# Kernel optimization log

Measured on AMD Instinct MI355X. Metric: run time of the kernel, lower is better.

## Reference

```python
import jax, jax.numpy as jnp
import numpy as np

EMBED_DIM = 1024
NUM_HEADS = 16
HEAD_DIM = EMBED_DIM // NUM_HEADS
SCALE = float(np.sqrt(HEAD_DIM))


def setup_inputs() -> dict:
    key = jax.random.key(0)
    ks = jax.random.split(key, 7)
    B, S, E = 2, 2048, EMBED_DIM
    query = jax.random.normal(ks[0], (B, S, E), dtype=jnp.float32)
    key_t = jax.random.normal(ks[1], (B, S, E), dtype=jnp.float32)
    value = jax.random.normal(ks[2], (B, S, E), dtype=jnp.float32)
    # nn.Linear(E, E, bias=False): weight shape (out, in); y = x @ W.T
    std = 1.0 / np.sqrt(E)
    Wq = jax.random.uniform(ks[3], (E, E), jnp.float32, -std, std)
    Wk = jax.random.uniform(ks[4], (E, E), jnp.float32, -std, std)
    Wv = jax.random.uniform(ks[5], (E, E), jnp.float32, -std, std)
    Wo = jax.random.uniform(ks[6], (E, E), jnp.float32, -std, std)
    return {"query": query, "key": key_t, "value": value,
            "Wq": Wq, "Wk": Wk, "Wv": Wv, "Wo": Wo}


def reference(query, key, value, Wq, Wk, Wv, Wo):
    B, S, E = query.shape
    H, D = NUM_HEADS, HEAD_DIM
    q = (query @ Wq.T).reshape(B, S, H, D).transpose(0, 2, 1, 3)  # [B,H,S,D]
    k = (key @ Wk.T).reshape(B, S, H, D).transpose(0, 2, 1, 3)
    v = (value @ Wv.T).reshape(B, S, H, D).transpose(0, 2, 1, 3)
    scores = jnp.einsum('bhqd,bhkd->bhqk', q, k) / SCALE  # [B,H,S,S]
    attn = jax.nn.softmax(scores, axis=-1)
    out = jnp.einsum('bhqk,bhkd->bhqd', attn, v)  # [B,H,S,D]
    out = out.transpose(0, 2, 1, 3).reshape(B, S, E)
    return out @ Wo.T
```

## Files before the change

### kernel.cpp

```cpp
#include <hip/hip_runtime.h>
#include <hip/hip_bf16.h>
#include <math.h>

typedef float f32x4 __attribute__((ext_vector_type(4)));
typedef __bf16 bf16x8 __attribute__((ext_vector_type(8)));
typedef unsigned short u16;
typedef u16 u16x8 __attribute__((ext_vector_type(8)));
typedef u16 u16x4 __attribute__((ext_vector_type(4)));
typedef unsigned ui32x4 __attribute__((ext_vector_type(4)));

__device__ __forceinline__ u16 f2bf(float f) {
    unsigned u = __builtin_bit_cast(unsigned, f);
    u = (u + 0x7fffu + ((u >> 16) & 1u)) >> 16;
    return (u16)u;
}
__device__ __forceinline__ unsigned cvtpk(float a, float b) {
    unsigned r;
    asm("v_cvt_pk_bf16_f32 %0, %1, %2" : "=v"(r) : "v"(a), "v"(b));
    return r;
}

#if __has_builtin(__builtin_amdgcn_exp2f)
#define EXP2(x) __builtin_amdgcn_exp2f(x)
#else
#define EXP2(x) exp2f(x)
#endif

__device__ __forceinline__ void gload16(const u16* g, u16* l) {
    __builtin_amdgcn_global_load_lds(
        (const __attribute__((address_space(1))) unsigned int*)(g),
        (__attribute__((address_space(3))) unsigned int*)(l), 16, 0, 0);
}

#if __has_builtin(__builtin_amdgcn_permlane32_swap) && __has_builtin(__builtin_amdgcn_permlane16_swap)
__device__ __forceinline__ void quad_swap(unsigned A, unsigned B, unsigned& dlo,
                                          unsigned& dhi, int quad) {
    auto t = __builtin_amdgcn_permlane32_swap(A, B, false, false);
    auto u = __builtin_amdgcn_permlane16_swap(t[0], t[1], false, false);
    dlo = u[0];
    dhi = u[1];
}
#else
__device__ __forceinline__ void quad_swap(unsigned A, unsigned B, unsigned& dlo,
                                          unsigned& dhi, int quad) {
    unsigned As = (unsigned)__shfl_xor((int)A, 32, 64);
    unsigned Bs = (unsigned)__shfl_xor((int)B, 32, 64);
    unsigned tx = (quad < 2) ? A : Bs;
    unsigned ty = (quad < 2) ? As : B;
    unsigned txs = (unsigned)__shfl_xor((int)tx, 16, 64);
    unsigned tys = (unsigned)__shfl_xor((int)ty, 16, 64);
    dlo = ((quad & 1) == 0) ? tx : tys;
    dhi = ((quad & 1) == 0) ? txs : ty;
}
#endif

__global__ __launch_bounds__(256) void cast_all(
    const float* __restrict__ q, const float* __restrict__ k, const float* __restrict__ v,
    const float* __restrict__ wq, const float* __restrict__ wk, const float* __restrict__ wv,
    const float* __restrict__ wo, u16* __restrict__ dst) {
    int i = blockIdx.x * 256 + threadIdx.x;
    const float* src;
    int off;
    if (i < 3145728) {
        int seg = i >> 20;
        src = (seg == 0) ? q : (seg == 1) ? k : v;
        off = i - (seg << 20);
    } else {
        int j = (i - 3145728) >> 18;
        src = (j == 0) ? wq : (j == 1) ? wk : (j == 2) ? wv : wo;
        off = (i - 3145728) - (j << 18);
    }
    float4 val = ((const float4*)src)[off];
    u16x4 o4;
    o4.x = f2bf(val.x); o4.y = f2bf(val.y); o4.z = f2bf(val.z); o4.w = f2bf(val.w);
    ((u16x4*)dst)[i] = o4;
}

__global__ __launch_bounds__(512) void qkv_gemm(
    const u16* __restrict__ Xq, const u16* __restrict__ Xk, const u16* __restrict__ Xv,
    const u16* __restrict__ Wq, const u16* __restrict__ Wk, const u16* __restrict__ Wv,
    u16* __restrict__ Qo, u16* __restrict__ Ko, u16* __restrict__ Vto) {
    constexpr int K = 1024;
    const int blk = blockIdx.x;
    const int mb = blk & 15;
    const int g = blk >> 4;
    const int z = g >> 3;
    const int nb = g & 7;
    const u16* __restrict__ A = (z == 0) ? Xq : (z == 1) ? Xk : Xv;
    const u16* __restrict__ W = (z == 0) ? Wq : (z == 1) ? Wk : Wv;
    u16* __restrict__ Out = (z == 0) ? Qo : (z == 1) ? Ko : Vto;

    __shared__ __align__(16) u16 Asm[2 * 256 * 64];
    __shared__ __align__(16) u16 Bsm[128 * 64];

    const int t = threadIdx.x;
    const int lane = t & 63, wave = t >> 6;
    const int quad = lane >> 4, c = lane & 15, cx = c & 7;
    const int wm = wave >> 1, wn = wave & 1;
    const int rowA0 = mb * 256;
    const int colB0 = nb * 128;

    const int l3 = lane >> 3, l7 = lane & 7;
    const int chs = (l7 ^ l3) << 3;
    const u16* gA[4];
    const u16* gB[2];
    int lbA[4];
    int lbB[2];
#pragma unroll
    for (int i = 0; i < 4; ++i) {
        int row = wave * 32 + i * 8 + l3;
        gA[i] = A + (size_t)(rowA0 + row) * K + chs;
        lbA[i] = (wave * 32 + i * 8) * 64;
    }
#pragma unroll
    for (int i = 0; i < 2; ++i) {
        int row = wave * 16 + i * 8 + l3;
        gB[i] = W + (size_t)(colB0 + row) * K + chs;
        lbB[i] = (wave * 16 + i * 8) * 64;
    }

    const f32x4 zero4 = {0.f, 0.f, 0.f, 0.f};
    f32x4 acc[4][4];
#pragma unroll
    for (int i = 0; i < 4; ++i)
#pragma unroll
        for (int j = 0; j < 4; ++j) acc[i][j] = zero4;

#pragma unroll
    for (int i = 0; i < 2; ++i) gload16(gB[i], Bsm + lbB[i]);
#pragma unroll
    for (int i = 0; i < 4; ++i) gload16(gA[i], Asm + lbA[i]);
#pragma unroll
    for (int i = 0; i < 4; ++i) gload16(gA[i] + 64, Asm + 16384 + lbA[i]);
    asm volatile("s_waitcnt vmcnt(4)" ::: "memory");
    __builtin_amdgcn_s_barrier();
    asm volatile("" ::: "memory");

    for (int kt = 0; kt < 16; ++kt) {
        const int cur = kt & 1;
        const u16* Ab = Asm + cur * 16384;
        const u16* Bb = Bsm;
#pragma unroll
        for (int ks = 0; ks < 2; ++ks) {
            const int co = ((ks * 4 + quad) ^ cx) << 3;
            bf16x8 af[4], bfr[4];
#pragma unroll
            for (int mi = 0; mi < 4; ++mi)
                af[mi] = *(const bf16x8*)(Ab + (wm * 64 + mi * 16 + c) * 64 + co);
#pragma unroll
            for (int nj = 0; nj < 4; ++nj)
                bfr[nj] = *(const bf16x8*)(Bb + (wn * 64 + nj * 16 + c) * 64 + co);
            if (ks == 1) {
                asm volatile("s_waitcnt lgkmcnt(0)" ::: "memory");
                __builtin_amdgcn_s_barrier();
                asm volatile("" ::: "memory");
                if (kt + 1 < 16) {
#pragma unroll
                    for (int i = 0; i < 2; ++i) gload16(gB[i] + (kt + 1) * 64, Bsm + lbB[i]);
                }
                if (kt + 2 < 16) {
                    const int koff = (kt + 2) * 64;
                    u16* ab = Asm + cur * 16384;
#pragma unroll
                    for (int i = 0; i < 4; ++i) gload16(gA[i] + koff, ab + lbA[i]);
                }
            }
            __builtin_amdgcn_s_setprio(1);
            if (z == 2) {
#pragma unroll
                for (int mi = 0; mi < 4; ++mi)
#pragma unroll
                    for (int nj = 0; nj < 4; ++nj)
                        acc[mi][nj] = __builtin_amdgcn_mfma_f32_16x16x32_bf16(bfr[nj], af[mi], acc[mi][nj], 0, 0, 0);
            } else {
#pragma unroll
                for (int mi = 0; mi < 4; ++mi)
#pragma unroll
                    for (int nj = 0; nj < 4; ++nj)
                        acc[mi][nj] = __builtin_amdgcn_mfma_f32_16x16x32_bf16(af[mi], bfr[nj], acc[mi][nj], 0, 0, 0);
            }
            __builtin_amdgcn_s_setprio(0);
        }
        if (kt <= 13) {
            asm volatile("s_waitcnt vmcnt(4)" ::: "memory");
        } else {
            asm volatile("s_waitcnt vmcnt(0)" ::: "memory");
        }
        __builtin_amdgcn_s_barrier();
        asm volatile("" ::: "memory");
    }

    const float scale = (z == 0) ? 0.18033688011112042f : 1.0f;
#pragma unroll
    for (int mi = 0; mi < 4; ++mi) {
#pragma unroll
        for (int nj = 0; nj < 4; ++nj) {
#pragma unroll
            for (int r = 0; r < 4; ++r) {
                float v = acc[mi][nj][r];
                if (z == 2) {
                    int n = colB0 + wn * 64 + nj * 16 + quad * 4 + r;
                    int m = rowA0 + wm * 64 + mi * 16 + c;
                    int b = m >> 11, s = m & 2047, h = n >> 6, d = n & 63;
                    Out[((((b << 4) | h) << 6) + d) * 2048 + s] = f2bf(v);
                } else {
                    int m = rowA0 + wm * 64 + mi * 16 + quad * 4 + r;
                    int n = colB0 + wn * 64 + nj * 16 + c;
                    int b = m >> 11, s = m & 2047, h = n >> 6, d = n & 63;
                    Out[((((b << 4) | h) * 2048 + s) << 6) + d] = f2bf(v * scale);
                }
            }
        }
    }
}

__global__ __launch_bounds__(512) void out_gemm(const u16* __restrict__ A,
                                                const u16* __restrict__ W,
                                                float* __restrict__ Out) {
    constexpr int K = 1024;
    __shared__ __align__(16) u16 Asm[2 * 128 * 64];
    __shared__ __align__(16) u16 Bsm[2 * 128 * 64];
    const int blk = blockIdx.x;
    const int mb = blk & 31;
    const int nb = blk >> 5;
    const int t = threadIdx.x;
    const int lane = t & 63, wave = t >> 6;
    const int quad = lane >> 4, c = lane & 15, cx = c & 7;
    const int wm = wave >> 2, wn = wave & 3;
    const int rowA0 = mb * 128;
    const int colB0 = nb * 128;

    const int l3 = lane >> 3, l7 = lane & 7;
    const int chs = (l7 ^ l3) << 3;
    const u16* gA[2];
    const u16* gB[2];
    int lb[2];
#pragma unroll
    for (int i = 0; i < 2; ++i) {
        int row = wave * 16 + i * 8 + l3;
        gA[i] = A + (size_t)(rowA0 + row) * K + chs;
        gB[i] = W + (size_t)(colB0 + row) * K + chs;
        lb[i] = (wave * 16 + i * 8) * 64;
    }

    const f32x4 zero4 = {0.f, 0.f, 0.f, 0.f};
    f32x4 acc[4][2];
#pragma unroll
    for (int i = 0; i < 4; ++i)
#pragma unroll
        for (int j = 0; j < 2; ++j) acc[i][j] = zero4;

#pragma unroll
    for (int i = 0; i < 2; ++i) {
        gload16(gA[i], Asm + lb[i]);
        gload16(gB[i], Bsm + lb[i]);
    }
#pragma unroll
    for (int i = 0; i < 2; ++i) {
        gload16(gA[i] + 64, Asm + 8192 + lb[i]);
        gload16(gB[i] + 64, Bsm + 8192 + lb[i]);
    }
    asm volatile("s_waitcnt vmcnt(4)" ::: "memory");
    __builtin_amdgcn_s_barrier();
    asm volatile("" ::: "memory");

    for (int kt = 0; kt < 16; ++kt) {
        const int cur = kt & 1;
        const u16* Ab = Asm + cur * 8192;
        const u16* Bb = Bsm + cur * 8192;
#pragma unroll
        for (int ks = 0; ks < 2; ++ks) {
            const int co = ((ks * 4 + quad) ^ cx) << 3;
            bf16x8 af[4], bfr[2];
#pragma unroll
            for (int mi = 0; mi < 4; ++mi)
                af[mi] = *(const bf16x8*)(Ab + (wm * 64 + mi * 16 + c) * 64 + co);
#pragma unroll
            for (int nj = 0; nj < 2; ++nj)
                bfr[nj] = *(const bf16x8*)(Bb + (wn * 32 + nj * 16 + c) * 64 + co);
            if (ks == 1) {
                asm volatile("s_waitcnt lgkmcnt(0)" ::: "memory");
                __builtin_amdgcn_s_barrier();
                asm volatile("" ::: "memory");
                if (kt + 2 < 16) {
                    const int koff = (kt + 2) * 64;
                    u16* ab = Asm + cur * 8192;
                    u16* bb = Bsm + cur * 8192;
#pragma unroll
                    for (int i = 0; i < 2; ++i) {
                        gload16(gA[i] + koff, ab + lb[i]);
                        gload16(gB[i] + koff, bb + lb[i]);
                    }
                }
            }
            __builtin_amdgcn_s_setprio(1);
#pragma unroll
            for (int mi = 0; mi < 4; ++mi)
#pragma unroll
                for (int nj = 0; nj < 2; ++nj)
                    acc[mi][nj] = __builtin_amdgcn_mfma_f32_16x16x32_bf16(af[mi], bfr[nj], acc[mi][nj], 0, 0, 0);
            __builtin_amdgcn_s_setprio(0);
        }
        if (kt <= 13) {
            asm volatile("s_waitcnt vmcnt(4)" ::: "memory");
        } else {
            asm volatile("s_waitcnt vmcnt(0)" ::: "memory");
        }
        __builtin_amdgcn_s_barrier();
        asm volatile("" ::: "memory");
    }

#pragma unroll
    for (int mi = 0; mi < 4; ++mi)
#pragma unroll
        for (int nj = 0; nj < 2; ++nj)
#pragma unroll
            for (int r = 0; r < 4; ++r) {
                int m = rowA0 + wm * 64 + mi * 16 + quad * 4 + r;
                int n = colB0 + wn * 32 + nj * 16 + c;
                Out[(m << 10) + n] = acc[mi][nj][r];
            }
}

__global__ __launch_bounds__(512, 4) void flash_attn(const u16* __restrict__ Qp,
                                                     const u16* __restrict__ Kp,
                                                     const u16* __restrict__ Vt,
                                                     u16* __restrict__ Ob) {
    constexpr int S = 2048;
    const int blk = blockIdx.x;
    const int j = blk & 31;
    const int bh = ((j & 7) << 2) | (j >> 3);
    const int b = bh >> 4, h = bh & 15;
    const int t = threadIdx.x, wave = t >> 6, lane = t & 63;
    const int wq = wave & 3, kh = wave >> 2;
    const int quad = lane >> 4, c = lane & 15, cx = c & 7;
    const int qw = (blk >> 5) * 128 + wq * 32;
    const u16* Qb = Qp + (bh * S + qw) * 64;
    const u16* Kb = Kp + (bh * S + kh * 1024) * 64;
    const u16* Vb = Vt + bh * 64 * S + kh * 1024;

    __shared__ __align__(16) u16 smem[32768];
    u16* const Kh = smem + kh * 8192;
    u16* const Vh = smem + 16384 + kh * 8192;

    bf16x8 qf[2][2];
#pragma unroll
    for (int qt = 0; qt < 2; ++qt)
#pragma unroll
        for (int hf = 0; hf < 2; ++hf)
            qf[qt][hf] = *(const bf16x8*)(Qb + (qt * 16 + c) * 64 + hf * 32 + quad * 8);

    u16x8 ou;
#pragma unroll
    for (int i = 0; i < 8; ++i) ou[i] = 0x3F80;
    const bf16x8 onesf = __builtin_bit_cast(bf16x8, ou);

    const int l3f = lane >> 3, l7f = lane & 7;
    const int chsf = (l7f ^ l3f) << 3;
    const u16* gK[2];
    const u16* gV[2];
    int lbase[2];
#pragma unroll
    for (int i = 0; i < 2; ++i) {
        int row = wq * 16 + i * 8 + l3f;
        gK[i] = Kb + row * 64 + chsf;
        gV[i] = Vb + row * 2048 + chsf;
        lbase[i] = (wq * 128 + i * 64) * 8;
    }
#pragma unroll
    for (int i = 0; i < 2; ++i) {
        gload16(gK[i], Kh + lbase[i]);
        gload16(gV[i], Vh + lbase[i]);
    }
    __syncthreads();

    const f32x4 zero4 = {0.f, 0.f, 0.f, 0.f};
    f32x4 o[2][4];
    f32x4 ol[2];
#pragma unroll
    for (int qt = 0; qt < 2; ++qt) {
        ol[qt] = zero4;
#pragma unroll
        for (int t2 = 0; t2 < 4; ++t2) o[qt][t2] = zero4;
    }

    const int co0 = (quad ^ cx) << 3, co1 = ((4 + quad) ^ cx) << 3;

    for (int it = 0; it < 16; ++it) {
        const int cur = it & 1;
        if (it + 1 < 16) {
#pragma unroll
            for (int i = 0; i < 2; ++i) {
                gload16(gK[i] + (it + 1) * 4096, Kh + (cur ^ 1) * 4096 + lbase[i]);
                gload16(gV[i] + (it + 1) * 64, Vh + (cur ^ 1) * 4096 + lbase[i]);
            }
        }
        const u16* Kc = Kh + cur * 4096;
        const u16* Vc = Vh + cur * 4096;
        f32x4 sc[4][2];
        __builtin_amdgcn_s_setprio(1);
#pragma unroll
        for (int kt = 0; kt < 4; ++kt) {
            const int krow = (kt * 16 + c) * 64;
            bf16x8 kf0 = *(const bf16x8*)(Kc + krow + co0);
            bf16x8 kf1 = *(const bf16x8*)(Kc + krow + co1);
#pragma unroll
            for (int qt = 0; qt < 2; ++qt) {
                f32x4 zz = zero4;
                zz = __builtin_amdgcn_mfma_f32_16x16x32_bf16(kf0, qf[qt][0], zz, 0, 0, 0);
                zz = __builtin_amdgcn_mfma_f32_16x16x32_bf16(kf1, qf[qt][1], zz, 0, 0, 0);
                sc[kt][qt] = zz;
            }
        }
        __builtin_amdgcn_s_setprio(0);
        bf16x8 af[2][2];
#pragma unroll
        for (int qt = 0; qt < 2; ++qt) {
            unsigned dw[4][2];
#pragma unroll
            for (int kt = 0; kt < 4; ++kt) {
                dw[kt][0] = cvtpk(EXP2(sc[kt][qt][0]), EXP2(sc[kt][qt][1]));
                dw[kt][1] = cvtpk(EXP2(sc[kt][qt][2]), EXP2(sc[kt][qt][3]));
            }
#pragma unroll
            for (int hh = 0; hh < 2; ++hh) {
                unsigned d0, d1, d2, d3;
                quad_swap(dw[2 * hh][0], dw[2 * hh + 1][0], d0, d2, quad);
                quad_swap(dw[2 * hh][1], dw[2 * hh + 1][1], d1, d3, quad);
                ui32x4 dd = {d0, d1, d2, d3};
                af[qt][hh] = __builtin_bit_cast(bf16x8, dd);
            }
        }
        __builtin_amdgcn_s_setprio(1);
#pragma unroll
        for (int qt = 0; qt < 2; ++qt) {
            ol[qt] = __builtin_amdgcn_mfma_f32_16x16x32_bf16(af[qt][0], onesf, ol[qt], 0, 0, 0);
            ol[qt] = __builtin_amdgcn_mfma_f32_16x16x32_bf16(af[qt][1], onesf, ol[qt], 0, 0, 0);
        }
#pragma unroll
        for (int t2 = 0; t2 < 4; ++t2) {
            const int vrow = (t2 * 16 + c) * 64;
            bf16x8 vf0 = *(const bf16x8*)(Vc + vrow + co0);
            bf16x8 vf1 = *(const bf16x8*)(Vc + vrow + co1);
#pragma unroll
            for (int qt = 0; qt < 2; ++qt) {
                o[qt][t2] = __builtin_amdgcn_mfma_f32_16x16x32_bf16(af[qt][0], vf0, o[qt][t2], 0, 0, 0);
                o[qt][t2] = __builtin_amdgcn_mfma_f32_16x16x32_bf16(af[qt][1], vf1, o[qt][t2], 0, 0, 0);
            }
        }
        __builtin_amdgcn_s_setprio(0);
        __syncthreads();
    }
    float* const cb = ((float*)smem) + ((wq << 6) | lane) * 41;
    if (kh == 1) {
        int idx = 0;
#pragma unroll
        for (int qt = 0; qt < 2; ++qt)
#pragma unroll
            for (int t2 = 0; t2 < 4; ++t2)
#pragma unroll
                for (int r = 0; r < 4; ++r) cb[idx++] = o[qt][t2][r];
#pragma unroll
        for (int qt = 0; qt < 2; ++qt)
#pragma unroll
            for (int r = 0; r < 4; ++r) cb[idx++] = ol[qt][r];
    }
    __syncthreads();
    if (kh == 0) {
        int idx = 0;
#pragma unroll
        for (int qt = 0; qt < 2; ++qt)
#pragma unroll
            for (int t2 = 0; t2 < 4; ++t2)
#pragma unroll
                for (int r = 0; r < 4; ++r) o[qt][t2][r] += cb[idx++];
#pragma unroll
        for (int qt = 0; qt < 2; ++qt)
#pragma unroll
            for (int r = 0; r < 4; ++r) ol[qt][r] += cb[idx++];
#pragma unroll
        for (int qt = 0; qt < 2; ++qt)
#pragma unroll
            for (int r = 0; r < 4; ++r) {
                float inv = 1.f / ol[qt][r];
                int row = qw + qt * 16 + quad * 4 + r;
                int base = ((b * S + row) * 16 + h) * 64;
#pragma unroll
                for (int t2 = 0; t2 < 4; ++t2)
                    Ob[base + t2 * 16 + c] = f2bf(o[qt][t2][r] * inv);
            }
    }
}

extern "C" void kernel_launch(void* const* d_in, const int* in_sizes, int n_in,
                              void* d_out, int out_size, void* d_ws, size_t ws_size,
                              hipStream_t stream) {
    const float* q  = (const float*)d_in[0];
    const float* k  = (const float*)d_in[1];
    const float* v  = (const float*)d_in[2];
    const float* wq = (const float*)d_in[3];
    const float* wk = (const float*)d_in[4];
    const float* wv = (const float*)d_in[5];
    const float* wo = (const float*)d_in[6];

    u16* ws = (u16*)d_ws;
    u16* qb  = ws;
    u16* kb  = ws + 4194304;
    u16* vb  = ws + 8388608;
    u16* wqb = ws + 12582912;
    u16* wkb = ws + 13631488;
    u16* wvb = ws + 14680064;
    u16* wob = ws + 15728640;
    u16* Qp  = ws + 16777216;
    u16* Kp  = ws + 20971520;
    u16* Vtp = ws + 25165824;
    u16* Obf = ws + 29360128;

    cast_all<<<16384, 256, 0, stream>>>(q, k, v, wq, wk, wv, wo, ws);

    qkv_gemm<<<384, 512, 0, stream>>>(qb, kb, vb, wqb, wkb, wvb, Qp, Kp, Vtp);

    flash_attn<<<512, 512, 0, stream>>>(Qp, Kp, Vtp, Obf);

    out_gemm<<<256, 512, 0, stream>>>(Obf, wob, (float*)d_out);
}
```

Before: 203.3 us.

## Fuse fp32-to-bf16 cast into QKV and output GEMM tile loads

Removes the separate cast kernel. The QKV GEMM and the Wo operand of the output GEMM now read fp32 directly from global memory, pack to bf16 in registers and store to LDS with a register-staged double buffer. The QKV GEMM tile shrinks from 256x128 to 128x128, doubling its grid, and the asynchronous global-to-LDS loads give way to synchronous register prefetch plus __syncthreads. This saves a full read and write pass over the inputs and weights, at the cost of reading fp32 (twice the bytes) inside the GEMMs and re-converting weights in every block.

```diff
diff --git a/kernel.cpp b/kernel.cpp
--- a/kernel.cpp
+++ b/kernel.cpp
@@ -6,17 +6,22 @@
 typedef __bf16 bf16x8 __attribute__((ext_vector_type(8)));
 typedef unsigned short u16;
 typedef u16 u16x8 __attribute__((ext_vector_type(8)));
-typedef u16 u16x4 __attribute__((ext_vector_type(4)));
 typedef unsigned ui32x4 __attribute__((ext_vector_type(4)));
 
+__device__ __forceinline__ unsigned cvtpk(float a, float b) {
+    unsigned r;
+    asm("v_cvt_pk_bf16_f32 %0, %1, %2" : "=v"(r) : "v"(a), "v"(b));
+    return r;
+}
 __device__ __forceinline__ u16 f2bf(float f) {
     unsigned u = __builtin_bit_cast(unsigned, f);
     u = (u + 0x7fffu + ((u >> 16) & 1u)) >> 16;
     return (u16)u;
 }
-__device__ __forceinline__ unsigned cvtpk(float a, float b) {
-    unsigned r;
-    asm("v_cvt_pk_bf16_f32 %0, %1, %2" : "=v"(r) : "v"(a), "v"(b));
+__device__ __forceinline__ ui32x4 pack8(float4 a, float4 b) {
+    ui32x4 r;
+    r.x = cvtpk(a.x, a.y); r.y = cvtpk(a.z, a.w);
+    r.z = cvtpk(b.x, b.y); r.w = cvtpk(b.z, b.w);
     return r;
 }
 
@@ -54,158 +59,130 @@
 }
 #endif
 
-__global__ __launch_bounds__(256) void cast_all(
-    const float* __restrict__ q, const float* __restrict__ k, const float* __restrict__ v,
-    const float* __restrict__ wq, const float* __restrict__ wk, const float* __restrict__ wv,
-    const float* __restrict__ wo, u16* __restrict__ dst) {
-    int i = blockIdx.x * 256 + threadIdx.x;
-    const float* src;
-    int off;
-    if (i < 3145728) {
-        int seg = i >> 20;
-        src = (seg == 0) ? q : (seg == 1) ? k : v;
-        off = i - (seg << 20);
-    } else {
-        int j = (i - 3145728) >> 18;
-        src = (j == 0) ? wq : (j == 1) ? wk : (j == 2) ? wv : wo;
-        off = (i - 3145728) - (j << 18);
-    }
-    float4 val = ((const float4*)src)[off];
-    u16x4 o4;
-    o4.x = f2bf(val.x); o4.y = f2bf(val.y); o4.z = f2bf(val.z); o4.w = f2bf(val.w);
-    ((u16x4*)dst)[i] = o4;
-}
-
 __global__ __launch_bounds__(512) void qkv_gemm(
-    const u16* __restrict__ Xq, const u16* __restrict__ Xk, const u16* __restrict__ Xv,
-    const u16* __restrict__ Wq, const u16* __restrict__ Wk, const u16* __restrict__ Wv,
+    const float* __restrict__ Xq, const float* __restrict__ Xk, const float* __restrict__ Xv,
+    const float* __restrict__ Wq, const float* __restrict__ Wk, const float* __restrict__ Wv,
     u16* __restrict__ Qo, u16* __restrict__ Ko, u16* __restrict__ Vto) {
-    constexpr int K = 1024;
     const int blk = blockIdx.x;
-    const int mb = blk & 15;
-    const int g = blk >> 4;
-    const int z = g >> 3;
-    const int nb = g & 7;
-    const u16* __restrict__ A = (z == 0) ? Xq : (z == 1) ? Xk : Xv;
-    const u16* __restrict__ W = (z == 0) ? Wq : (z == 1) ? Wk : Wv;
+    const int mb = blk & 31;
+    const int nb = (blk >> 5) & 7;
+    const int z = blk >> 8;
+    const float* __restrict__ A = (z == 0) ? Xq : (z == 1) ? Xk : Xv;
+    const float* __restrict__ W = (z == 0) ? Wq : (z == 1) ? Wk : Wv;
     u16* __restrict__ Out = (z == 0) ? Qo : (z == 1) ? Ko : Vto;
 
-    __shared__ __align__(16) u16 Asm[2 * 256 * 64];
-    __shared__ __align__(16) u16 Bsm[128 * 64];
+    __shared__ __align__(16) u16 Asm[2 * 128 * 64];
+    __shared__ __align__(16) u16 Bsm[2 * 128 * 64];
 
     const int t = threadIdx.x;
     const int lane = t & 63, wave = t >> 6;
     const int quad = lane >> 4, c = lane & 15, cx = c & 7;
-    const int wm = wave >> 1, wn = wave & 1;
-    const int rowA0 = mb * 256;
+    const int wm = wave >> 2, wn = wave & 3;
+    const int rowA0 = mb * 128;
     const int colB0 = nb * 128;
 
     const int l3 = lane >> 3, l7 = lane & 7;
-    const int chs = (l7 ^ l3) << 3;
-    const u16* gA[4];
-    const u16* gB[2];
-    int lbA[4];
-    int lbB[2];
-#pragma unroll
-    for (int i = 0; i < 4; ++i) {
-        int row = wave * 32 + i * 8 + l3;
-        gA[i] = A + (size_t)(rowA0 + row) * K + chs;
-        lbA[i] = (wave * 32 + i * 8) * 64;
-    }
+    const float* gA[2];
+    const float* gB[2];
+    int lb[2];
 #pragma unroll
     for (int i = 0; i < 2; ++i) {
         int row = wave * 16 + i * 8 + l3;
-        gB[i] = W + (size_t)(colB0 + row) * K + chs;
-        lbB[i] = (wave * 16 + i * 8) * 64;
+        gA[i] = A + (size_t)(rowA0 + row) * 1024 + ((l7 ^ l3) << 3);
+        gB[i] = W + (size_t)(colB0 + row) * 1024 + ((l7 ^ l3) << 3);
+        lb[i] = (wave * 16 + i * 8) * 64 + lane * 8;
     }
 
     const f32x4 zero4 = {0.f, 0.f, 0.f, 0.f};
-    f32x4 acc[4][4];
+    f32x4 acc[4][2];
 #pragma unroll
     for (int i = 0; i < 4; ++i)
 #pragma unroll
-        for (int j = 0; j < 4; ++j) acc[i][j] = zero4;
-
-#pragma unroll
-    for (int i = 0; i < 2; ++i) gload16(gB[i], Bsm + lbB[i]);
-#pragma unroll
-    for (int i = 0; i < 4; ++i) gload16(gA[i], Asm + lbA[i]);
-#pragma unroll
-    for (int i = 0; i < 4; ++i) gload16(gA[i] + 64, Asm + 16384 + lbA[i]);
-    asm volatile("s_waitcnt vmcnt(4)" ::: "memory");
-    __builtin_amdgcn_s_barrier();
-    asm volatile("" ::: "memory");
+        for (int j = 0; j < 2; ++j) acc[i][j] = zero4;
+
+    float4 pa[2][2], pb[2][2];
+#pragma unroll
+    for (int i = 0; i < 2; ++i) {
+        pa[i][0] = ((const float4*)gA[i])[0];
+        pa[i][1] = ((const float4*)gA[i])[1];
+        pb[i][0] = ((const float4*)gB[i])[0];
+        pb[i][1] = ((const float4*)gB[i])[1];
+    }
+#pragma unroll
+    for (int i = 0; i < 2; ++i) {
+        *(ui32x4*)(Asm + lb[i]) = pack8(pa[i][0], pa[i][1]);
+        *(ui32x4*)(Bsm + lb[i]) = pack8(pb[i][0], pb[i][1]);
+    }
+    __syncthreads();
 
     for (int kt = 0; kt < 16; ++kt) {
         const int cur = kt & 1;
-        const u16* Ab = Asm + cur * 16384;
-        const u16* Bb = Bsm;
+        if (kt + 1 < 16) {
+            const int koff = (kt + 1) * 64;
+#pragma unroll
+            for (int i = 0; i < 2; ++i) {
+                pa[i][0] = ((const float4*)(gA[i] + koff))[0];
+                pa[i][1] = ((const float4*)(gA[i] + koff))[1];
+                pb[i][0] = ((const float4*)(gB[i] + koff))[0];
+                pb[i][1] = ((const float4*)(gB[i] + koff))[1];
+            }
+        }
+        const u16* Ab = Asm + cur * 8192;
+        const u16* Bb = Bsm + cur * 8192;
 #pragma unroll
         for (int ks = 0; ks < 2; ++ks) {
             const int co = ((ks * 4 + quad) ^ cx) << 3;
-            bf16x8 af[4], bfr[4];
+            bf16x8 af[4], bfr[2];
 #pragma unroll
             for (int mi = 0; mi < 4; ++mi)
                 af[mi] = *(const bf16x8*)(Ab + (wm * 64 + mi * 16 + c) * 64 + co);
 #pragma unroll
-            for (int nj = 0; nj < 4; ++nj)
-                bfr[nj] = *(const bf16x8*)(Bb + (wn * 64 + nj * 16 + c) * 64 + co);
-            if (ks == 1) {
-                asm volatile("s_waitcnt lgkmcnt(0)" ::: "memory");
-                __builtin_amdgcn_s_barrier();
-                asm volatile("" ::: "memory");
-                if (kt + 1 < 16) {
-#pragma unroll
-                    for (int i = 0; i < 2; ++i) gload16(gB[i] + (kt + 1) * 64, Bsm + lbB[i]);
-                }
-                if (kt + 2 < 16) {
-                    const int koff = (kt + 2) * 64;
-                    u16* ab = Asm + cur * 16384;
-#pragma unroll
-                    for (int i = 0; i < 4; ++i) gload16(gA[i] + koff, ab + lbA[i]);
-                }
-            }
+            for (int nj = 0; nj < 2; ++nj)
+                bfr[nj] = *(const bf16x8*)(Bb + (wn * 32 + nj * 16 + c) * 64 + co);
             __builtin_amdgcn_s_setprio(1);
             if (z == 2) {
 #pragma unroll
                 for (int mi = 0; mi < 4; ++mi)
 #pragma unroll
-                    for (int nj = 0; nj < 4; ++nj)
+                    for (int nj = 0; nj < 2; ++nj)
                         acc[mi][nj] = __builtin_amdgcn_mfma_f32_16x16x32_bf16(bfr[nj], af[mi], acc[mi][nj], 0, 0, 0);
             } else {
 #pragma unroll
                 for (int mi = 0; mi < 4; ++mi)
 #pragma unroll
-                    for (int nj = 0; nj < 4; ++nj)
+                    for (int nj = 0; nj < 2; ++nj)
                         acc[mi][nj] = __builtin_amdgcn_mfma_f32_16x16x32_bf16(af[mi], bfr[nj], acc[mi][nj], 0, 0, 0);
             }
             __builtin_amdgcn_s_setprio(0);
         }
-        if (kt <= 13) {
-            asm volatile("s_waitcnt vmcnt(4)" ::: "memory");
-        } else {
-            asm volatile("s_waitcnt vmcnt(0)" ::: "memory");
-        }
-        __builtin_amdgcn_s_barrier();
-        asm volatile("" ::: "memory");
+        if (kt + 1 < 16) {
+            u16* an = Asm + (cur ^ 1) * 8192;
+            u16* bn = Bsm + (cur ^ 1) * 8192;
+#pragma unroll
+            for (int i = 0; i < 2; ++i) {
+                *(ui32x4*)(an + lb[i]) = pack8(pa[i][0], pa[i][1]);
+                *(ui32x4*)(bn + lb[i]) = pack8(pb[i][0], pb[i][1]);
+            }
+        }
+        __syncthreads();
     }
 
     const float scale = (z == 0) ? 0.18033688011112042f : 1.0f;
 #pragma unroll
     for (int mi = 0; mi < 4; ++mi) {
 #pragma unroll
-        for (int nj = 0; nj < 4; ++nj) {
+        for (int nj = 0; nj < 2; ++nj) {
 #pragma unroll
             for (int r = 0; r < 4; ++r) {
                 float v = acc[mi][nj][r];
                 if (z == 2) {
-                    int n = colB0 + wn * 64 + nj * 16 + quad * 4 + r;
+                    int n = colB0 + wn * 32 + nj * 16 + quad * 4 + r;
                     int m = rowA0 + wm * 64 + mi * 16 + c;
                     int b = m >> 11, s = m & 2047, h = n >> 6, d = n & 63;
                     Out[((((b << 4) | h) << 6) + d) * 2048 + s] = f2bf(v);
                 } else {
                     int m = rowA0 + wm * 64 + mi * 16 + quad * 4 + r;
-                    int n = colB0 + wn * 64 + nj * 16 + c;
+                    int n = colB0 + wn * 32 + nj * 16 + c;
                     int b = m >> 11, s = m & 2047, h = n >> 6, d = n & 63;
                     Out[((((b << 4) | h) * 2048 + s) << 6) + d] = f2bf(v * scale);
                 }
@@ -215,9 +192,8 @@
 }
 
 __global__ __launch_bounds__(512) void out_gemm(const u16* __restrict__ A,
-                                                const u16* __restrict__ W,
+                                                const float* __restrict__ W,
                                                 float* __restrict__ Out) {
-    constexpr int K = 1024;
     __shared__ __align__(16) u16 Asm[2 * 128 * 64];
     __shared__ __align__(16) u16 Bsm[2 * 128 * 64];
     const int blk = blockIdx.x;
@@ -233,14 +209,16 @@
     const int l3 = lane >> 3, l7 = lane & 7;
     const int chs = (l7 ^ l3) << 3;
     const u16* gA[2];
-    const u16* gB[2];
-    int lb[2];
+    const float* gB[2];
+    int lbA[2];
+    int lbB[2];
 #pragma unroll
     for (int i = 0; i < 2; ++i) {
         int row = wave * 16 + i * 8 + l3;
-        gA[i] = A + (size_t)(rowA0 + row) * K + chs;
-        gB[i] = W + (size_t)(colB0 + row) * K + chs;
-        lb[i] = (wave * 16 + i * 8) * 64;
+        gA[i] = A + (size_t)(rowA0 + row) * 1024 + chs;
+        gB[i] = W + (size_t)(colB0 + row) * 1024 + ((l7 ^ l3) << 3);
+        lbA[i] = (wave * 16 + i * 8) * 64;
+        lbB[i] = (wave * 16 + i * 8) * 64 + lane * 8;
     }
 
     const f32x4 zero4 = {0.f, 0.f, 0.f, 0.f};
@@ -250,22 +228,29 @@
 #pragma unroll
         for (int j = 0; j < 2; ++j) acc[i][j] = zero4;
 
-#pragma unroll
-    for (int i = 0; i < 2; ++i) {
-        gload16(gA[i], Asm + lb[i]);
-        gload16(gB[i], Bsm + lb[i]);
-    }
-#pragma unroll
-    for (int i = 0; i < 2; ++i) {
-        gload16(gA[i] + 64, Asm + 8192 + lb[i]);
-        gload16(gB[i] + 64, Bsm + 8192 + lb[i]);
-    }
-    asm volatile("s_waitcnt vmcnt(4)" ::: "memory");
-    __builtin_amdgcn_s_barrier();
-    asm volatile("" ::: "memory");
+    float4 pb[2][2];
+#pragma unroll
+    for (int i = 0; i < 2; ++i) {
+        gload16(gA[i], Asm + lbA[i]);
+        pb[i][0] = ((const float4*)gB[i])[0];
+        pb[i][1] = ((const float4*)gB[i])[1];
+    }
+#pragma unroll
+    for (int i = 0; i < 2; ++i) *(ui32x4*)(Bsm + lbB[i]) = pack8(pb[i][0], pb[i][1]);
+    __syncthreads();
 
     for (int kt = 0; kt < 16; ++kt) {
         const int cur = kt & 1;
+        if (kt + 1 < 16) {
+            const int koff = (kt + 1) * 64;
+            u16* an = Asm + (cur ^ 1) * 8192;
+#pragma unroll
+            for (int i = 0; i < 2; ++i) {
+                gload16(gA[i] + koff, an + lbA[i]);
+                pb[i][0] = ((const float4*)(gB[i] + koff))[0];
+                pb[i][1] = ((const float4*)(gB[i] + koff))[1];
+            }
+        }
         const u16* Ab = Asm + cur * 8192;
         const u16* Bb = Bsm + cur * 8192;
 #pragma unroll
@@ -278,21 +263,6 @@
 #pragma unroll
             for (int nj = 0; nj < 2; ++nj)
                 bfr[nj] = *(const bf16x8*)(Bb + (wn * 32 + nj * 16 + c) * 64 + co);
-            if (ks == 1) {
-                asm volatile("s_waitcnt lgkmcnt(0)" ::: "memory");
-                __builtin_amdgcn_s_barrier();
-                asm volatile("" ::: "memory");
-                if (kt + 2 < 16) {
-                    const int koff = (kt + 2) * 64;
-                    u16* ab = Asm + cur * 8192;
-                    u16* bb = Bsm + cur * 8192;
-#pragma unroll
-                    for (int i = 0; i < 2; ++i) {
-                        gload16(gA[i] + koff, ab + lb[i]);
-                        gload16(gB[i] + koff, bb + lb[i]);
-                    }
-                }
-            }
             __builtin_amdgcn_s_setprio(1);
 #pragma unroll
             for (int mi = 0; mi < 4; ++mi)
@@ -301,13 +271,12 @@
                     acc[mi][nj] = __builtin_amdgcn_mfma_f32_16x16x32_bf16(af[mi], bfr[nj], acc[mi][nj], 0, 0, 0);
             __builtin_amdgcn_s_setprio(0);
         }
-        if (kt <= 13) {
-            asm volatile("s_waitcnt vmcnt(4)" ::: "memory");
-        } else {
-            asm volatile("s_waitcnt vmcnt(0)" ::: "memory");
-        }
-        __builtin_amdgcn_s_barrier();
-        asm volatile("" ::: "memory");
+        if (kt + 1 < 16) {
+            u16* bn = Bsm + (cur ^ 1) * 8192;
+#pragma unroll
+            for (int i = 0; i < 2; ++i) *(ui32x4*)(bn + lbB[i]) = pack8(pb[i][0], pb[i][1]);
+        }
+        __syncthreads();
     }
 
 #pragma unroll
@@ -504,23 +473,14 @@
     const float* wo = (const float*)d_in[6];
 
     u16* ws = (u16*)d_ws;
-    u16* qb  = ws;
-    u16* kb  = ws + 4194304;
-    u16* vb  = ws + 8388608;
-    u16* wqb = ws + 12582912;
-    u16* wkb = ws + 13631488;
-    u16* wvb = ws + 14680064;
-    u16* wob = ws + 15728640;
-    u16* Qp  = ws + 16777216;
-    u16* Kp  = ws + 20971520;
-    u16* Vtp = ws + 25165824;
-    u16* Obf = ws + 29360128;
-
-    cast_all<<<16384, 256, 0, stream>>>(q, k, v, wq, wk, wv, wo, ws);
-
-    qkv_gemm<<<384, 512, 0, stream>>>(qb, kb, vb, wqb, wkb, wvb, Qp, Kp, Vtp);
+    u16* Qp  = ws;
+    u16* Kp  = ws + 4194304;
+    u16* Vtp = ws + 8388608;
+    u16* Obf = ws + 12582912;
+
+    qkv_gemm<<<768, 512, 0, stream>>>(q, k, v, wq, wk, wv, Qp, Kp, Vtp);
 
     flash_attn<<<512, 512, 0, stream>>>(Qp, Kp, Vtp, Obf);
 
-    out_gemm<<<256, 512, 0, stream>>>(Obf, wob, (float*)d_out);
-}
+    out_gemm<<<256, 512, 0, stream>>>(Obf, wo, (float*)d_out);
+}
```

New measurement: 227.5 us. 1.12x slower.
